# Kernel tuning notes

Hardware: AMD Instinct MI355X
Metric: run time of the kernel (lower is better)

Reference implementation:

```python
import jax, jax.numpy as jnp
import numpy as np

C = 128
GROUPS = 8
EPS = 1e-5


def setup_inputs() -> dict:
    key = jax.random.key(0)
    ks = jax.random.split(key, 7)
    B, D, H, W = 2, 8, 32, 32
    x = jax.random.normal(ks[0], (B, C, D, H, W), dtype=jnp.float32)
    gamma = jnp.ones((C,), dtype=jnp.float32)
    beta = jnp.zeros((C,), dtype=jnp.float32)
    w_qkv = jax.random.normal(ks[1], (3 * C, C), dtype=jnp.float32) * 0.02
    b_qkv = jnp.zeros((3 * C,), dtype=jnp.float32)
    w_proj = jax.random.normal(ks[2], (C, C), dtype=jnp.float32) * 0.02
    b_proj = jnp.zeros((C,), dtype=jnp.float32)
    return {"x": x, "gamma": gamma, "beta": beta, "w_qkv": w_qkv,
            "b_qkv": b_qkv, "w_proj": w_proj, "b_proj": b_proj}


def _group_norm(x, gamma, beta):
    B, Cc, D, H, W = x.shape
    xg = x.reshape(B, GROUPS, Cc // GROUPS, D, H, W)
    mean = jnp.mean(xg, axis=(2, 3, 4, 5), keepdims=True)
    var = jnp.var(xg, axis=(2, 3, 4, 5), keepdims=True)
    xn = (xg - mean) * jax.lax.rsqrt(var + EPS)
    xn = xn.reshape(B, Cc, D, H, W)
    return xn * gamma[None, :, None, None, None] + beta[None, :, None, None, None]


def reference(x, gamma, beta, w_qkv, b_qkv, w_proj, b_proj):
    B, Cc, D, H, W = x.shape
    N = D * H * W
    h = _group_norm(x, gamma, beta)
    # 1x1x1 conv == per-voxel matmul over channels
    qkv = jnp.einsum('bcdhw,oc->bodhw', h, w_qkv) + b_qkv[None, :, None, None, None]
    q, k, v = jnp.split(qkv, 3, axis=1)  # each [B, C, D, H, W]
    q = q.reshape(B, Cc, N).transpose(0, 2, 1)  # [B, N, C]
    k = k.reshape(B, Cc, N).transpose(0, 2, 1)
    v = v.reshape(B, Cc, N).transpose(0, 2, 1)
    scale = Cc ** (-0.5)
    attn = jax.nn.softmax(jnp.einsum('bnc,bmc->bnm', q, k) * scale, axis=-1)
    h = jnp.einsum('bnm,bmc->bnc', attn, v)  # [B, N, C]
    h = h.transpose(0, 2, 1).reshape(B, Cc, D, H, W)
    out = jnp.einsum('bcdhw,oc->bodhw', h, w_proj) + b_proj[None, :, None, None, None]
    return x + out
```

## Files before the change

kernel.cpp:

```cpp
#include <hip/hip_runtime.h>

typedef __bf16 bf16x8 __attribute__((ext_vector_type(8)));
typedef float  f32x4  __attribute__((ext_vector_type(4)));
typedef float  f32x16 __attribute__((ext_vector_type(16)));
typedef float  f32x2  __attribute__((ext_vector_type(2)));
typedef unsigned int uint32;
typedef unsigned int u32x2 __attribute__((ext_vector_type(2)));
typedef int i32x4 __attribute__((ext_vector_type(4)));
typedef int i32x8 __attribute__((ext_vector_type(8)));
typedef long long i64;
typedef long long i64x4v __attribute__((ext_vector_type(4)));

#define MFMA16(a, b, c) __builtin_amdgcn_mfma_f32_16x16x32_bf16((a), (b), (c), 0, 0, 0)
#define MFMA32F8(a, b, c) __builtin_amdgcn_mfma_f32_32x32x16_fp8_fp8((a), (b), (c), 0, 0, 0)
#define GLL(gsrc, ldst) __builtin_amdgcn_global_load_lds( \
    (const __attribute__((address_space(1))) uint32*)(gsrc), \
    (__attribute__((address_space(3))) uint32*)(ldst), 16, 0, 0)

static constexpr int Cch = 128;
static constexpr int Nvox = 8192;

__device__ inline f32x16 mx4(i32x8 a, i32x8 b, f32x16 c) {
#if __has_builtin(__builtin_amdgcn_mfma_scale_f32_32x32x64_f8f6f4)
  return __builtin_amdgcn_mfma_scale_f32_32x32x64_f8f6f4(
      a, b, c, 0 , 0 ,
      0, 0x7F7F7F7Fu, 0, 0x7F7F7F7Fu );
#else
  i64x4v av = __builtin_bit_cast(i64x4v, a);
  i64x4v bv = __builtin_bit_cast(i64x4v, b);
  c = MFMA32F8(av[0], bv[0], c);
  c = MFMA32F8(av[1], bv[1], c);
  c = MFMA32F8(av[2], bv[2], c);
  c = MFMA32F8(av[3], bv[3], c);
  return c;
#endif
}

__device__ inline unsigned int pkbf(float x, float y) {
  unsigned short ux = __builtin_bit_cast(unsigned short, (__bf16)x);
  unsigned short uy = __builtin_bit_cast(unsigned short, (__bf16)y);
  return (unsigned int)ux | ((unsigned int)uy << 16);
}

__device__ inline unsigned int pk4fp8(float a, float b, float c, float d) {
  int w = 0;
  w = __builtin_amdgcn_cvt_pk_fp8_f32(a, b, w, false);
  w = __builtin_amdgcn_cvt_pk_fp8_f32(c, d, w, true);
  return (unsigned int)w;
}
__device__ inline unsigned char fp8b(float x) {
  return (unsigned char)(__builtin_amdgcn_cvt_pk_fp8_f32(x, x, 0, false) & 0xff);
}

__device__ inline void lane32_swap(unsigned int& x, unsigned int& y) {
#if __has_builtin(__builtin_amdgcn_permlane32_swap)
  auto r = __builtin_amdgcn_permlane32_swap(x, y, false, false);
  x = r[0]; y = r[1];
#else
  unsigned int sx = (unsigned int)__shfl_xor((int)x, 32);
  unsigned int sy = (unsigned int)__shfl_xor((int)y, 32);
  bool lo = ((threadIdx.x & 63) < 32);
  unsigned int nx = lo ? x : sy;
  unsigned int ny = lo ? sx : y;
  x = nx; y = ny;
#endif
}
__device__ inline float red32_sum(float v) {
  unsigned int a = __builtin_bit_cast(unsigned int, v), b = a;
  lane32_swap(a, b);
  return __builtin_bit_cast(float, a) + __builtin_bit_cast(float, b);
}

__global__ __launch_bounds__(256) void gn_part_k(const float* __restrict__ x,
                                                 f32x2* __restrict__ part,
                                                 const float* __restrict__ wq,
                                                 const float* __restrict__ wp,
                                                 __bf16* __restrict__ wqb,
                                                 __bf16* __restrict__ wpb) {
  int wi = blockIdx.x * 256 + threadIdx.x;
  if (wi < 49152) wqb[wi] = (__bf16)wq[wi];
  else wpb[wi - 49152] = (__bf16)wp[wi - 49152];

  int bg = blockIdx.x >> 4, pt = blockIdx.x & 15;
  const f32x4* xb = (const f32x4*)(x + (size_t)bg * 131072 + (size_t)pt * 8192);
  float s = 0.f, ss = 0.f;
  for (int i = threadIdx.x; i < 2048; i += 256) {
    f32x4 v = xb[i];
    s += (v.x + v.y) + (v.z + v.w);
    ss += (v.x * v.x + v.y * v.y) + (v.z * v.z + v.w * v.w);
  }
#pragma unroll
  for (int off = 32; off; off >>= 1) {
    s  += __shfl_down(s, off);
    ss += __shfl_down(ss, off);
  }
  __shared__ float rb[4], rbss[4];
  if ((threadIdx.x & 63) == 0) { rb[threadIdx.x >> 6] = s; rbss[threadIdx.x >> 6] = ss; }
  __syncthreads();
  if (threadIdx.x == 0) {
    f32x2 o; o.x = rb[0] + rb[1] + rb[2] + rb[3];
    o.y = rbss[0] + rbss[1] + rbss[2] + rbss[3];
    part[blockIdx.x] = o;
  }
}

__global__ __launch_bounds__(256) void gn_apply_k(const float* __restrict__ x,
                                                  const float* __restrict__ gamma,
                                                  const float* __restrict__ beta,
                                                  const f32x2* __restrict__ part,
                                                  __bf16* __restrict__ xn) {
  __shared__ __bf16 t[64][136];
  __shared__ float sm_mean[16], sm_rstd[16];
  int tid = threadIdx.x;
  {
    f32x2 v = part[tid];
    float s = v.x, ss = v.y;
#pragma unroll
    for (int off = 1; off < 16; off <<= 1) {
      s += __shfl_xor(s, off);
      ss += __shfl_xor(ss, off);
    }
    if ((tid & 15) == 0) {
      int bg = tid >> 4;
      const float invn = 1.f / 131072.f;
      float mean = s * invn;
      float var = ss * invn - mean * mean;
      sm_mean[bg] = mean;
      sm_rstd[bg] = rsqrtf(var + 1e-5f);
    }
  }
  __syncthreads();
  int b = blockIdx.x >> 7;
  int n0 = (blockIdx.x & 127) << 6;
  const float* xb = x + (size_t)b * Cch * Nvox;
  for (int i = threadIdx.x; i < 128 * 64; i += 256) {
    int c = i >> 6, nl = i & 63;
    int g = c >> 4;
    float mean = sm_mean[b * 8 + g];
    float rstd = sm_rstd[b * 8 + g];
    float v = xb[(size_t)c * Nvox + n0 + nl];
    t[nl][c] = (__bf16)((v - mean) * rstd * gamma[c] + beta[c]);
  }
  __syncthreads();
  __bf16* outb = xn + (size_t)b * Nvox * Cch;
  for (int i = threadIdx.x; i < 64 * 16; i += 256) {
    int row = i >> 4, ch = (i & 15) << 3;
    *reinterpret_cast<bf16x8*>(&outb[(size_t)(n0 + row) * Cch + ch]) =
        *reinterpret_cast<const bf16x8*>(&t[row][ch]);
  }
}

__global__ __launch_bounds__(256) void qkv_k(const __bf16* __restrict__ xn,
                                             const __bf16* __restrict__ wq,
                                             const float* __restrict__ b_qkv,
                                             unsigned char* __restrict__ q8,
                                             unsigned char* __restrict__ k8,
                                             unsigned char* __restrict__ v8t) {
  int id = blockIdx.x;
  int b = id / 768;
  int rr = id % 768;
  int o0b = (rr >> 7) * 64;
  int n0 = (rr & 127) * 64;
  int w = threadIdx.x >> 6, l = threadIdx.x & 63;
  int lr = l & 15, lh = l >> 4;
  int ow = o0b + w * 16;
  const float k2 = 0.08838834764831845f * 1.4426950408889634f;

  bf16x8 a[4];
#pragma unroll
  for (int kc = 0; kc < 4; kc++)
    a[kc] = *reinterpret_cast<const bf16x8*>(&wq[(size_t)(ow + lr) * 128 + kc * 32 + lh * 8]);

  const __bf16* xb = xn + (size_t)b * Nvox * Cch;
#pragma unroll
  for (int ns = 0; ns < 4; ns++) {
    f32x4 acc = {0.f, 0.f, 0.f, 0.f};
#pragma unroll
    for (int kc = 0; kc < 4; kc++) {
      bf16x8 bf = *reinterpret_cast<const bf16x8*>(
          &xb[(size_t)(n0 + ns * 16 + lr) * Cch + kc * 32 + lh * 8]);
      acc = MFMA16(a[kc], bf, acc);
    }
    int o0 = ow + lh * 4;
    int n = n0 + ns * 16 + lr;
    float f0 = acc[0] + b_qkv[o0 + 0];
    float f1 = acc[1] + b_qkv[o0 + 1];
    float f2 = acc[2] + b_qkv[o0 + 2];
    float f3 = acc[3] + b_qkv[o0 + 3];
    if (o0 < 128) {
      *reinterpret_cast<unsigned int*>(
          q8 + ((size_t)b * Nvox + n) * 128 + o0) =
          pk4fp8(f0 * k2, f1 * k2, f2 * k2, f3 * k2);
    } else if (o0 < 256) {
      *reinterpret_cast<unsigned int*>(
          k8 + ((size_t)b * Nvox + n) * 128 + (o0 - 128)) = pk4fp8(f0, f1, f2, f3);
    } else {
      int c0 = o0 - 256;
      int kk = n & 63;
      int r4 = kk & 15;
      int hh = (r4 >> 2) & 1;
      int jj = (r4 & 3) + (((r4 >> 3) & 1) << 2);
      int m = ((kk >> 5) << 5) + (hh << 4) + (((kk >> 4) & 1) << 3) + jj;
      int nst = (n & ~63) | m;
      v8t[((size_t)b * Cch + c0 + 0) * Nvox + nst] = fp8b(f0);
      v8t[((size_t)b * Cch + c0 + 1) * Nvox + nst] = fp8b(f1);
      v8t[((size_t)b * Cch + c0 + 2) * Nvox + nst] = fp8b(f2);
      v8t[((size_t)b * Cch + c0 + 3) * Nvox + nst] = fp8b(f3);
    }
  }
}

__global__ __launch_bounds__(256, 2) void attn_k(const unsigned char* __restrict__ q,
                                                 const unsigned char* __restrict__ kk,
                                                 const unsigned char* __restrict__ vt,
                                                 __bf16* __restrict__ po0,
                                                 __bf16* __restrict__ po1,
                                                 __bf16* __restrict__ po2,
                                                 __bf16* __restrict__ po3,
                                                 f32x2* __restrict__ ml) {
  extern __shared__ char smem[];
  const int bi = blockIdx.x;
  const int kq = bi & 3;
  const int b = (bi >> 2) & 1;
  const int qgrp = bi >> 3;
  const int w = threadIdx.x >> 6;
  const int l = threadIdx.x & 63;
  const int l31 = l & 31, h = l >> 5;
  const int swl16 = (l31 & 15) << 4;

  const char* kbase = (const char*)kk + ((size_t)b * 8192 + (size_t)kq * 2048) * 128;
  const char* vbase = (const char*)vt + (size_t)b * 1048576 + (size_t)kq * 2048;

  const unsigned char* qrow = q +
      ((size_t)b * 8192 + (size_t)qgrp * 128 + (size_t)w * 32 + l31) * 128 + h * 32;
  i32x8 qa8[2];
#pragma unroll
  for (int dc = 0; dc < 2; dc++) {
    i32x4 q0 = *reinterpret_cast<const i32x4*>(qrow + dc * 64);
    i32x4 q1 = *reinterpret_cast<const i32x4*>(qrow + dc * 64 + 16);
    qa8[dc] = __builtin_shufflevector(q0, q1, 0, 1, 2, 3, 4, 5, 6, 7);
  }

  f32x16 O[4];
#pragma unroll
  for (int cb = 0; cb < 4; cb++)
#pragma unroll
    for (int r = 0; r < 16; r++) O[cb][r] = 0.f;
  float s0 = 0.f, s1 = 0.f, s2 = 0.f, s3 = 0.f;

  auto stage = [&](int t, int bs) {
    if (w < 2) {
      const char* kt = kbase + (size_t)t * 64 * 128;
      char* dst = smem + bs * 16384;
#pragma unroll
      for (int it = 0; it < 4; ++it) {
        int ob = (w * 4 + it) * 1024;
        int o = ob + l * 16;
        int row = o >> 8;
        int lcol = (o & 255) ^ ((row & 15) << 4);
        int ksel = lcol >> 7, c = lcol & 127;
        GLL(kt + (size_t)(ksel * 32 + row) * 128 + c, dst + ob);
      }
    } else {
      const char* vtile = vbase + (size_t)t * 64;
      char* dst = smem + bs * 16384 + 8192;
#pragma unroll
      for (int it = 0; it < 4; ++it) {
        int ob = ((w - 2) * 4 + it) * 1024;
        int o = ob + l * 16;
        int row = o >> 8;
        int lcol = (o & 255) ^ ((row & 15) << 4);
        int cs = lcol >> 6, k16 = lcol & 63;
        GLL(vtile + (size_t)(cs * 32 + row) * 8192 + k16, dst + ob);
      }
    }
  };

  stage(0, 0);
  int cur = 0;
  const int NT = 32;

  for (int t = 0; t < NT; ++t) {
    asm volatile("s_waitcnt vmcnt(0) lgkmcnt(0)" ::: "memory");
    __builtin_amdgcn_sched_barrier(0);
    __syncthreads();
    if (t + 1 < NT) stage(t + 1, cur ^ 1);

    const char* Kb = smem + cur * 16384;
    const char* Vb = Kb + 8192;

    f32x16 St[2];
#pragma unroll
    for (int ks = 0; ks < 2; ks++)
#pragma unroll
      for (int r = 0; r < 16; r++) St[ks][r] = 0.f;
    __builtin_amdgcn_s_setprio(1);
#pragma unroll
    for (int ks = 0; ks < 2; ks++) {
#pragma unroll
      for (int dc = 0; dc < 2; dc++) {
        int base = ks * 128 + dc * 64 + h * 32;
        i32x4 k0 = *reinterpret_cast<const i32x4*>(
            Kb + (size_t)l31 * 256 + (base ^ swl16));
        i32x4 k1 = *reinterpret_cast<const i32x4*>(
            Kb + (size_t)l31 * 256 + ((base + 16) ^ swl16));
        St[ks] = mx4(__builtin_shufflevector(k0, k1, 0, 1, 2, 3, 4, 5, 6, 7),
                     qa8[dc], St[ks]);
      }
    }
    __builtin_amdgcn_s_setprio(0);

#pragma unroll
    for (int ks = 0; ks < 2; ks++)
#pragma unroll
      for (int r = 0; r < 16; r++)
        St[ks][r] = __builtin_amdgcn_exp2f(St[ks][r]);
#pragma unroll
    for (int ks = 0; ks < 2; ks++)
#pragma unroll
      for (int r = 0; r < 16; r += 4) {
        s0 += St[ks][r + 0]; s1 += St[ks][r + 1];
        s2 += St[ks][r + 2]; s3 += St[ks][r + 3];
      }

    i32x8 pb;
#pragma unroll
    for (int ks = 0; ks < 2; ks++) {
      pb[ks * 4 + 0] = (int)pk4fp8(St[ks][0],  St[ks][1],  St[ks][2],  St[ks][3]);
      pb[ks * 4 + 1] = (int)pk4fp8(St[ks][4],  St[ks][5],  St[ks][6],  St[ks][7]);
      pb[ks * 4 + 2] = (int)pk4fp8(St[ks][8],  St[ks][9],  St[ks][10], St[ks][11]);
      pb[ks * 4 + 3] = (int)pk4fp8(St[ks][12], St[ks][13], St[ks][14], St[ks][15]);
    }

    __builtin_amdgcn_s_setprio(1);
#pragma unroll
    for (int cb = 0; cb < 4; cb++) {
      int vb0 = cb * 64 + h * 16;
      i32x4 v0 = *reinterpret_cast<const i32x4*>(
          Vb + (size_t)l31 * 256 + (vb0 ^ swl16));
      i32x4 v1 = *reinterpret_cast<const i32x4*>(
          Vb + (size_t)l31 * 256 + ((vb0 + 32) ^ swl16));
      O[cb] = mx4(__builtin_shufflevector(v0, v1, 0, 1, 2, 3, 4, 5, 6, 7),
                  pb, O[cb]);
    }
    __builtin_amdgcn_s_setprio(0);
    cur ^= 1;
  }

  float lsum = red32_sum((s0 + s1) + (s2 + s3));
  __bf16* po = (kq == 0) ? po0 : (kq == 1) ? po1 : (kq == 2) ? po2 : po3;
  int qg = b * 8192 + qgrp * 128 + w * 32 + l31;
#pragma unroll
  for (int cb = 0; cb < 4; cb++) {
#pragma unroll
    for (int rq = 0; rq < 4; rq++) {
      int c = cb * 32 + rq * 8 + h * 4;
      u32x2 wv;
      wv[0] = pkbf(O[cb][rq * 4 + 0], O[cb][rq * 4 + 1]);
      wv[1] = pkbf(O[cb][rq * 4 + 2], O[cb][rq * 4 + 3]);
      *reinterpret_cast<u32x2*>((char*)po + ((size_t)qg * 128 + c) * 2) = wv;
    }
  }
  if (l < 32) {
    f32x2 v; v.x = 0.f; v.y = lsum;
    ml[(size_t)kq * 16384 + qg] = v;
  }
}

__global__ __launch_bounds__(256) void proj_k(const __bf16* __restrict__ po0,
                                              const __bf16* __restrict__ po1,
                                              const __bf16* __restrict__ po2,
                                              const __bf16* __restrict__ po3,
                                              const f32x2* __restrict__ ml,
                                              const __bf16* __restrict__ wp,
                                              const float* __restrict__ b_proj,
                                              const float* __restrict__ x,
                                              float* __restrict__ out) {
  int id = blockIdx.x;
  int b = id >> 8;
  int co0 = ((id >> 7) & 1) * 64;
  int n0 = (id & 127) * 64;
  int w = threadIdx.x >> 6, l = threadIdx.x & 63;
  int lr = l & 15, lh = l >> 4;
  int cow = co0 + w * 16;

  bf16x8 a[4];
#pragma unroll
  for (int kc = 0; kc < 4; kc++)
    a[kc] = *reinterpret_cast<const bf16x8*>(&wp[(size_t)(cow + lr) * 128 + kc * 32 + lh * 8]);

#pragma unroll
  for (int ns = 0; ns < 4; ns++) {
    int n = n0 + ns * 16 + lr;
    int qg = b * 8192 + n;
    f32x2 a0 = ml[qg], a1 = ml[16384 + qg], a2 = ml[32768 + qg], a3 = ml[49152 + qg];
    float M = fmaxf(fmaxf(a0.x, a1.x), fmaxf(a2.x, a3.x));
    float e0 = __builtin_amdgcn_exp2f(a0.x - M);
    float e1 = __builtin_amdgcn_exp2f(a1.x - M);
    float e2 = __builtin_amdgcn_exp2f(a2.x - M);
    float e3 = __builtin_amdgcn_exp2f(a3.x - M);
    float invL = 1.f / (e0 * a0.y + e1 * a1.y + e2 * a2.y + e3 * a3.y);
    float c0f = e0 * invL, c1f = e1 * invL, c2f = e2 * invL, c3f = e3 * invL;

    f32x4 acc = {0.f, 0.f, 0.f, 0.f};
#pragma unroll
    for (int kc = 0; kc < 4; kc++) {
      size_t off = (size_t)qg * 128 + kc * 32 + lh * 8;
      bf16x8 v0 = *reinterpret_cast<const bf16x8*>(&po0[off]);
      bf16x8 v1 = *reinterpret_cast<const bf16x8*>(&po1[off]);
      bf16x8 v2 = *reinterpret_cast<const bf16x8*>(&po2[off]);
      bf16x8 v3 = *reinterpret_cast<const bf16x8*>(&po3[off]);
      bf16x8 hv;
#pragma unroll
      for (int i = 0; i < 8; i++)
        hv[i] = (__bf16)(c0f * (float)v0[i] + c1f * (float)v1[i] +
                         c2f * (float)v2[i] + c3f * (float)v3[i]);
      acc = MFMA16(a[kc], hv, acc);
    }
#pragma unroll
    for (int r2 = 0; r2 < 4; r2++) {
      int co = cow + lh * 4 + r2;
      size_t idx = ((size_t)b * Cch + co) * Nvox + n;
      out[idx] = x[idx] + b_proj[co] + acc[r2];
    }
  }
}

extern "C" void kernel_launch(void* const* d_in, const int* in_sizes, int n_in,
                              void* d_out, int out_size, void* d_ws, size_t ws_size,
                              hipStream_t stream) {
  const float* x      = (const float*)d_in[0];
  const float* gamma  = (const float*)d_in[1];
  const float* beta   = (const float*)d_in[2];
  const float* w_qkv  = (const float*)d_in[3];
  const float* b_qkv  = (const float*)d_in[4];
  const float* w_proj = (const float*)d_in[5];
  const float* b_proj = (const float*)d_in[6];
  float* out = (float*)d_out;

  char* ws = (char*)d_ws;
  f32x2*  part  = (f32x2*)(ws + 256);
  __bf16* wq_b  = (__bf16*)(ws + 4096);
  __bf16* wp_b  = (__bf16*)(ws + 4096 + 98304);
  size_t base = 135168;
  const size_t SZ = (size_t)2 * Nvox * Cch * sizeof(__bf16);
  __bf16* xn  = (__bf16*)(ws + base + 0 * SZ);
  unsigned char* q8  = (unsigned char*)(ws + base + 1 * SZ);
  unsigned char* k8  = (unsigned char*)(ws + base + 2 * SZ);
  unsigned char* v8t = (unsigned char*)(ws + base + 3 * SZ);
  __bf16* hw  = (__bf16*)(ws + base + 4 * SZ);
  f32x2*  ml  = (f32x2*)(ws + base + 5 * SZ);
  __bf16* po2 = (__bf16*)(ws + base + 5 * SZ + 524288);
  __bf16* po3 = (__bf16*)(ws + base + 5 * SZ + 524288 + SZ);

  (void)hipFuncSetAttribute((const void*)attn_k,
                            hipFuncAttributeMaxDynamicSharedMemorySize, 32768);

  gn_part_k<<<256, 256, 0, stream>>>(x, part, w_qkv, w_proj, wq_b, wp_b);
  gn_apply_k<<<256, 256, 0, stream>>>(x, gamma, beta, part, xn);
  qkv_k<<<1536, 256, 0, stream>>>(xn, wq_b, b_qkv, q8, k8, v8t);
  attn_k<<<512, 256, 32768, stream>>>(q8, k8, v8t, hw, xn, po2, po3, ml);
  proj_k<<<512, 256, 0, stream>>>(hw, xn, po2, po3, ml, wp_b, b_proj, x, out);
}
```

Baseline: 92.97 us.

## Stage V transpose through LDS in qkv and double attention key tile per sync

In the QKV projection kernel, the V output is first gathered into a shared-memory 64x64 tile and then written to global memory as 16-byte row segments, replacing scattered single-byte stores. This targets the cost of uncoalesced byte writes. The attention kernel now stages 128 keys per barrier instead of 64, processing two sub-tiles per loop iteration and halving the number of synchronisations and waits. The price is double the LDS (64 KB per block), which may lower occupancy under the launch bound of two blocks.

```diff
diff --git a/kernel.cpp b/kernel.cpp
--- a/kernel.cpp
+++ b/kernel.cpp
@@ -6,6 +6,7 @@
 typedef float  f32x2  __attribute__((ext_vector_type(2)));
 typedef unsigned int uint32;
 typedef unsigned int u32x2 __attribute__((ext_vector_type(2)));
+typedef unsigned int u32x4 __attribute__((ext_vector_type(4)));
 typedef int i32x4 __attribute__((ext_vector_type(4)));
 typedef int i32x8 __attribute__((ext_vector_type(8)));
 typedef long long i64;
@@ -156,6 +157,7 @@
                                              unsigned char* __restrict__ q8,
                                              unsigned char* __restrict__ k8,
                                              unsigned char* __restrict__ v8t) {
+  __shared__ unsigned char vtl[64][64];
   int id = blockIdx.x;
   int b = id / 768;
   int rr = id % 768;
@@ -187,26 +189,33 @@
     float f1 = acc[1] + b_qkv[o0 + 1];
     float f2 = acc[2] + b_qkv[o0 + 2];
     float f3 = acc[3] + b_qkv[o0 + 3];
-    if (o0 < 128) {
+    if (o0b < 128) {
       *reinterpret_cast<unsigned int*>(
           q8 + ((size_t)b * Nvox + n) * 128 + o0) =
           pk4fp8(f0 * k2, f1 * k2, f2 * k2, f3 * k2);
-    } else if (o0 < 256) {
+    } else if (o0b < 256) {
       *reinterpret_cast<unsigned int*>(
           k8 + ((size_t)b * Nvox + n) * 128 + (o0 - 128)) = pk4fp8(f0, f1, f2, f3);
     } else {
-      int c0 = o0 - 256;
+      int crel = w * 16 + lh * 4;
       int kk = n & 63;
       int r4 = kk & 15;
       int hh = (r4 >> 2) & 1;
       int jj = (r4 & 3) + (((r4 >> 3) & 1) << 2);
       int m = ((kk >> 5) << 5) + (hh << 4) + (((kk >> 4) & 1) << 3) + jj;
-      int nst = (n & ~63) | m;
-      v8t[((size_t)b * Cch + c0 + 0) * Nvox + nst] = fp8b(f0);
-      v8t[((size_t)b * Cch + c0 + 1) * Nvox + nst] = fp8b(f1);
-      v8t[((size_t)b * Cch + c0 + 2) * Nvox + nst] = fp8b(f2);
-      v8t[((size_t)b * Cch + c0 + 3) * Nvox + nst] = fp8b(f3);
-    }
+      vtl[crel + 0][m] = fp8b(f0);
+      vtl[crel + 1][m] = fp8b(f1);
+      vtl[crel + 2][m] = fp8b(f2);
+      vtl[crel + 3][m] = fp8b(f3);
+    }
+  }
+  if (o0b >= 256) {
+    __syncthreads();
+    int cbase = o0b - 256;
+    int row = threadIdx.x >> 2, seg = threadIdx.x & 3;
+    *reinterpret_cast<u32x4*>(
+        v8t + ((size_t)b * Cch + cbase + row) * Nvox + n0 + seg * 16) =
+        *reinterpret_cast<const u32x4*>(&vtl[row][seg * 16]);
   }
 }
 
@@ -250,11 +259,11 @@
 
   auto stage = [&](int t, int bs) {
     if (w < 2) {
-      const char* kt = kbase + (size_t)t * 64 * 128;
-      char* dst = smem + bs * 16384;
-#pragma unroll
-      for (int it = 0; it < 4; ++it) {
-        int ob = (w * 4 + it) * 1024;
+      const char* kt = kbase + (size_t)t * 16384 + (size_t)w * 8192;
+      char* dst = smem + bs * 32768 + w * 8192;
+#pragma unroll
+      for (int it = 0; it < 8; ++it) {
+        int ob = it * 1024;
         int o = ob + l * 16;
         int row = o >> 8;
         int lcol = (o & 255) ^ ((row & 15) << 4);
@@ -262,11 +271,11 @@
         GLL(kt + (size_t)(ksel * 32 + row) * 128 + c, dst + ob);
       }
     } else {
-      const char* vtile = vbase + (size_t)t * 64;
-      char* dst = smem + bs * 16384 + 8192;
-#pragma unroll
-      for (int it = 0; it < 4; ++it) {
-        int ob = ((w - 2) * 4 + it) * 1024;
+      const char* vtile = vbase + (size_t)t * 128 + (w - 2) * 64;
+      char* dst = smem + bs * 32768 + 16384 + (w - 2) * 8192;
+#pragma unroll
+      for (int it = 0; it < 8; ++it) {
+        int ob = it * 1024;
         int o = ob + l * 16;
         int row = o >> 8;
         int lcol = (o & 255) ^ ((row & 15) << 4);
@@ -278,7 +287,7 @@
 
   stage(0, 0);
   int cur = 0;
-  const int NT = 32;
+  const int NT = 16;
 
   for (int t = 0; t < NT; ++t) {
     asm volatile("s_waitcnt vmcnt(0) lgkmcnt(0)" ::: "memory");
@@ -286,64 +295,68 @@
     __syncthreads();
     if (t + 1 < NT) stage(t + 1, cur ^ 1);
 
-    const char* Kb = smem + cur * 16384;
-    const char* Vb = Kb + 8192;
-
-    f32x16 St[2];
-#pragma unroll
-    for (int ks = 0; ks < 2; ks++)
-#pragma unroll
-      for (int r = 0; r < 16; r++) St[ks][r] = 0.f;
-    __builtin_amdgcn_s_setprio(1);
-#pragma unroll
-    for (int ks = 0; ks < 2; ks++) {
-#pragma unroll
-      for (int dc = 0; dc < 2; dc++) {
-        int base = ks * 128 + dc * 64 + h * 32;
-        i32x4 k0 = *reinterpret_cast<const i32x4*>(
-            Kb + (size_t)l31 * 256 + (base ^ swl16));
-        i32x4 k1 = *reinterpret_cast<const i32x4*>(
-            Kb + (size_t)l31 * 256 + ((base + 16) ^ swl16));
-        St[ks] = mx4(__builtin_shufflevector(k0, k1, 0, 1, 2, 3, 4, 5, 6, 7),
-                     qa8[dc], St[ks]);
+    const char* buf = smem + cur * 32768;
+#pragma unroll
+    for (int ss = 0; ss < 2; ++ss) {
+      const char* Kb = buf + ss * 8192;
+      const char* Vb = buf + 16384 + ss * 8192;
+
+      f32x16 St[2];
+#pragma unroll
+      for (int ks = 0; ks < 2; ks++)
+#pragma unroll
+        for (int r = 0; r < 16; r++) St[ks][r] = 0.f;
+      __builtin_amdgcn_s_setprio(1);
+#pragma unroll
+      for (int ks = 0; ks < 2; ks++) {
+#pragma unroll
+        for (int dc = 0; dc < 2; dc++) {
+          int base = ks * 128 + dc * 64 + h * 32;
+          i32x4 k0 = *reinterpret_cast<const i32x4*>(
+              Kb + (size_t)l31 * 256 + (base ^ swl16));
+          i32x4 k1 = *reinterpret_cast<const i32x4*>(
+              Kb + (size_t)l31 * 256 + ((base + 16) ^ swl16));
+          St[ks] = mx4(__builtin_shufflevector(k0, k1, 0, 1, 2, 3, 4, 5, 6, 7),
+                       qa8[dc], St[ks]);
+        }
       }
-    }
-    __builtin_amdgcn_s_setprio(0);
-
-#pragma unroll
-    for (int ks = 0; ks < 2; ks++)
-#pragma unroll
-      for (int r = 0; r < 16; r++)
-        St[ks][r] = __builtin_amdgcn_exp2f(St[ks][r]);
-#pragma unroll
-    for (int ks = 0; ks < 2; ks++)
-#pragma unroll
-      for (int r = 0; r < 16; r += 4) {
-        s0 += St[ks][r + 0]; s1 += St[ks][r + 1];
-        s2 += St[ks][r + 2]; s3 += St[ks][r + 3];
+      __builtin_amdgcn_s_setprio(0);
+
+#pragma unroll
+      for (int ks = 0; ks < 2; ks++)
+#pragma unroll
+        for (int r = 0; r < 16; r++)
+          St[ks][r] = __builtin_amdgcn_exp2f(St[ks][r]);
+#pragma unroll
+      for (int ks = 0; ks < 2; ks++)
+#pragma unroll
+        for (int r = 0; r < 16; r += 4) {
+          s0 += St[ks][r + 0]; s1 += St[ks][r + 1];
+          s2 += St[ks][r + 2]; s3 += St[ks][r + 3];
+        }
+
+      i32x8 pb;
+#pragma unroll
+      for (int ks = 0; ks < 2; ks++) {
+        pb[ks * 4 + 0] = (int)pk4fp8(St[ks][0],  St[ks][1],  St[ks][2],  St[ks][3]);
+        pb[ks * 4 + 1] = (int)pk4fp8(St[ks][4],  St[ks][5],  St[ks][6],  St[ks][7]);
+        pb[ks * 4 + 2] = (int)pk4fp8(St[ks][8],  St[ks][9],  St[ks][10], St[ks][11]);
+        pb[ks * 4 + 3] = (int)pk4fp8(St[ks][12], St[ks][13], St[ks][14], St[ks][15]);
       }
 
-    i32x8 pb;
-#pragma unroll
-    for (int ks = 0; ks < 2; ks++) {
-      pb[ks * 4 + 0] = (int)pk4fp8(St[ks][0],  St[ks][1],  St[ks][2],  St[ks][3]);
-      pb[ks * 4 + 1] = (int)pk4fp8(St[ks][4],  St[ks][5],  St[ks][6],  St[ks][7]);
-      pb[ks * 4 + 2] = (int)pk4fp8(St[ks][8],  St[ks][9],  St[ks][10], St[ks][11]);
-      pb[ks * 4 + 3] = (int)pk4fp8(St[ks][12], St[ks][13], St[ks][14], St[ks][15]);
-    }
-
-    __builtin_amdgcn_s_setprio(1);
-#pragma unroll
-    for (int cb = 0; cb < 4; cb++) {
-      int vb0 = cb * 64 + h * 16;
-      i32x4 v0 = *reinterpret_cast<const i32x4*>(
-          Vb + (size_t)l31 * 256 + (vb0 ^ swl16));
-      i32x4 v1 = *reinterpret_cast<const i32x4*>(
-          Vb + (size_t)l31 * 256 + ((vb0 + 32) ^ swl16));
-      O[cb] = mx4(__builtin_shufflevector(v0, v1, 0, 1, 2, 3, 4, 5, 6, 7),
-                  pb, O[cb]);
-    }
-    __builtin_amdgcn_s_setprio(0);
+      __builtin_amdgcn_s_setprio(1);
+#pragma unroll
+      for (int cb = 0; cb < 4; cb++) {
+        int vb0 = cb * 64 + h * 16;
+        i32x4 v0 = *reinterpret_cast<const i32x4*>(
+            Vb + (size_t)l31 * 256 + (vb0 ^ swl16));
+        i32x4 v1 = *reinterpret_cast<const i32x4*>(
+            Vb + (size_t)l31 * 256 + ((vb0 + 32) ^ swl16));
+        O[cb] = mx4(__builtin_shufflevector(v0, v1, 0, 1, 2, 3, 4, 5, 6, 7),
+                    pb, O[cb]);
+      }
+      __builtin_amdgcn_s_setprio(0);
+    }
     cur ^= 1;
   }
 
@@ -454,11 +467,11 @@
   __bf16* po3 = (__bf16*)(ws + base + 5 * SZ + 524288 + SZ);
 
   (void)hipFuncSetAttribute((const void*)attn_k,
-                            hipFuncAttributeMaxDynamicSharedMemorySize, 32768);
+                            hipFuncAttributeMaxDynamicSharedMemorySize, 65536);
 
   gn_part_k<<<256, 256, 0, stream>>>(x, part, w_qkv, w_proj, wq_b, wp_b);
   gn_apply_k<<<256, 256, 0, stream>>>(x, gamma, beta, part, xn);
   qkv_k<<<1536, 256, 0, stream>>>(xn, wq_b, b_qkv, q8, k8, v8t);
-  attn_k<<<512, 256, 32768, stream>>>(q8, k8, v8t, hw, xn, po2, po3, ml);
+  attn_k<<<512, 256, 65536, stream>>>(q8, k8, v8t, hw, xn, po2, po3, ml);
   proj_k<<<512, 256, 0, stream>>>(hw, xn, po2, po3, ml, wp_b, b_proj, x, out);
 }
```

Result: no change. 92.87 us (-0.1%).

## Stage xn tile in LDS, loop all QKV outputs per block, coalesce V stores

Applied to the files above, without the earlier changes.

The QKV kernel now loads each 64-voxel activation tile into shared memory once and iterates over all six 64-wide output tiles within one block, instead of launching a separate block per output tile that re-reads xn from global memory. The transposed V output is first staged in a shared buffer and then written with 16-byte coalesced stores, replacing scattered single-byte global writes. The grid shrinks from 1536 to 256 blocks, which lowers parallelism and occupancy on a large GPU and adds extra barriers.

```diff
diff --git a/kernel.cpp b/kernel.cpp
--- a/kernel.cpp
+++ b/kernel.cpp
@@ -6,6 +6,7 @@
 typedef float  f32x2  __attribute__((ext_vector_type(2)));
 typedef unsigned int uint32;
 typedef unsigned int u32x2 __attribute__((ext_vector_type(2)));
+typedef unsigned int u32x4 __attribute__((ext_vector_type(4)));
 typedef int i32x4 __attribute__((ext_vector_type(4)));
 typedef int i32x8 __attribute__((ext_vector_type(8)));
 typedef long long i64;
@@ -156,56 +157,77 @@
                                              unsigned char* __restrict__ q8,
                                              unsigned char* __restrict__ k8,
                                              unsigned char* __restrict__ v8t) {
+  __shared__ __bf16 xt[64][136];
+  __shared__ unsigned char vtl[64][64];
   int id = blockIdx.x;
-  int b = id / 768;
-  int rr = id % 768;
-  int o0b = (rr >> 7) * 64;
-  int n0 = (rr & 127) * 64;
+  int b = id >> 7;
+  int n0 = (id & 127) * 64;
   int w = threadIdx.x >> 6, l = threadIdx.x & 63;
   int lr = l & 15, lh = l >> 4;
-  int ow = o0b + w * 16;
   const float k2 = 0.08838834764831845f * 1.4426950408889634f;
 
-  bf16x8 a[4];
-#pragma unroll
-  for (int kc = 0; kc < 4; kc++)
-    a[kc] = *reinterpret_cast<const bf16x8*>(&wq[(size_t)(ow + lr) * 128 + kc * 32 + lh * 8]);
-
-  const __bf16* xb = xn + (size_t)b * Nvox * Cch;
-#pragma unroll
-  for (int ns = 0; ns < 4; ns++) {
-    f32x4 acc = {0.f, 0.f, 0.f, 0.f};
-#pragma unroll
-    for (int kc = 0; kc < 4; kc++) {
-      bf16x8 bf = *reinterpret_cast<const bf16x8*>(
-          &xb[(size_t)(n0 + ns * 16 + lr) * Cch + kc * 32 + lh * 8]);
-      acc = MFMA16(a[kc], bf, acc);
-    }
-    int o0 = ow + lh * 4;
-    int n = n0 + ns * 16 + lr;
-    float f0 = acc[0] + b_qkv[o0 + 0];
-    float f1 = acc[1] + b_qkv[o0 + 1];
-    float f2 = acc[2] + b_qkv[o0 + 2];
-    float f3 = acc[3] + b_qkv[o0 + 3];
-    if (o0 < 128) {
-      *reinterpret_cast<unsigned int*>(
-          q8 + ((size_t)b * Nvox + n) * 128 + o0) =
-          pk4fp8(f0 * k2, f1 * k2, f2 * k2, f3 * k2);
-    } else if (o0 < 256) {
-      *reinterpret_cast<unsigned int*>(
-          k8 + ((size_t)b * Nvox + n) * 128 + (o0 - 128)) = pk4fp8(f0, f1, f2, f3);
-    } else {
-      int c0 = o0 - 256;
-      int kk = n & 63;
-      int r4 = kk & 15;
-      int hh = (r4 >> 2) & 1;
-      int jj = (r4 & 3) + (((r4 >> 3) & 1) << 2);
-      int m = ((kk >> 5) << 5) + (hh << 4) + (((kk >> 4) & 1) << 3) + jj;
-      int nst = (n & ~63) | m;
-      v8t[((size_t)b * Cch + c0 + 0) * Nvox + nst] = fp8b(f0);
-      v8t[((size_t)b * Cch + c0 + 1) * Nvox + nst] = fp8b(f1);
-      v8t[((size_t)b * Cch + c0 + 2) * Nvox + nst] = fp8b(f2);
-      v8t[((size_t)b * Cch + c0 + 3) * Nvox + nst] = fp8b(f3);
+  const __bf16* xb = xn + ((size_t)b * Nvox + n0) * Cch;
+  for (int i = threadIdx.x; i < 64 * 16; i += 256) {
+    int row = i >> 4, ch = (i & 15) << 3;
+    *reinterpret_cast<bf16x8*>(&xt[row][ch]) =
+        *reinterpret_cast<const bf16x8*>(&xb[(size_t)row * Cch + ch]);
+  }
+  __syncthreads();
+
+#pragma unroll
+  for (int ot = 0; ot < 6; ++ot) {
+    int o0b = ot * 64;
+    int ow = o0b + w * 16;
+    bf16x8 a[4];
+#pragma unroll
+    for (int kc = 0; kc < 4; kc++)
+      a[kc] = *reinterpret_cast<const bf16x8*>(
+          &wq[(size_t)(ow + lr) * 128 + kc * 32 + lh * 8]);
+
+#pragma unroll
+    for (int ns = 0; ns < 4; ns++) {
+      f32x4 acc = {0.f, 0.f, 0.f, 0.f};
+#pragma unroll
+      for (int kc = 0; kc < 4; kc++) {
+        bf16x8 bf = *reinterpret_cast<const bf16x8*>(
+            &xt[ns * 16 + lr][kc * 32 + lh * 8]);
+        acc = MFMA16(a[kc], bf, acc);
+      }
+      int o0 = ow + lh * 4;
+      int n = n0 + ns * 16 + lr;
+      float f0 = acc[0] + b_qkv[o0 + 0];
+      float f1 = acc[1] + b_qkv[o0 + 1];
+      float f2 = acc[2] + b_qkv[o0 + 2];
+      float f3 = acc[3] + b_qkv[o0 + 3];
+      if (ot < 2) {
+        *reinterpret_cast<unsigned int*>(
+            q8 + ((size_t)b * Nvox + n) * 128 + o0) =
+            pk4fp8(f0 * k2, f1 * k2, f2 * k2, f3 * k2);
+      } else if (ot < 4) {
+        *reinterpret_cast<unsigned int*>(
+            k8 + ((size_t)b * Nvox + n) * 128 + (o0 - 128)) =
+            pk4fp8(f0, f1, f2, f3);
+      } else {
+        int crel = w * 16 + lh * 4;
+        int kk = ns * 16 + lr;
+        int r4 = kk & 15;
+        int hh = (r4 >> 2) & 1;
+        int jj = (r4 & 3) + (((r4 >> 3) & 1) << 2);
+        int m = ((kk >> 5) << 5) + (hh << 4) + (((kk >> 4) & 1) << 3) + jj;
+        vtl[crel + 0][m] = fp8b(f0);
+        vtl[crel + 1][m] = fp8b(f1);
+        vtl[crel + 2][m] = fp8b(f2);
+        vtl[crel + 3][m] = fp8b(f3);
+      }
+    }
+    if (ot >= 4) {
+      __syncthreads();
+      int cbase = (ot - 4) * 64;
+      int row = threadIdx.x >> 2, seg = threadIdx.x & 3;
+      *reinterpret_cast<u32x4*>(
+          v8t + ((size_t)b * Cch + cbase + row) * Nvox + n0 + seg * 16) =
+          *reinterpret_cast<const u32x4*>(&vtl[row][seg * 16]);
+      __syncthreads();
     }
   }
 }
@@ -458,7 +480,7 @@
 
   gn_part_k<<<256, 256, 0, stream>>>(x, part, w_qkv, w_proj, wq_b, wp_b);
   gn_apply_k<<<256, 256, 0, stream>>>(x, gamma, beta, part, xn);
-  qkv_k<<<1536, 256, 0, stream>>>(xn, wq_b, b_qkv, q8, k8, v8t);
+  qkv_k<<<256, 256, 0, stream>>>(xn, wq_b, b_qkv, q8, k8, v8t);
   attn_k<<<512, 256, 32768, stream>>>(q8, k8, v8t, hw, xn, po2, po3, ml);
   proj_k<<<512, 256, 0, stream>>>(hw, xn, po2, po3, ml, wp_b, b_proj, x, out);
 }
```

Result: faster. 86.00 us, median of 2 (-7.5%).
